# Optimization experiments

Measured on AMD Instinct MI355X. Metric: run time of the kernel, lower is better.

The kernel has to match this reference:

```python
import jax, jax.numpy as jnp
import numpy as np

TAU = 2.0
V_TH = 1.0


def setup_inputs() -> dict:
    key = jax.random.key(0)
    k1, k2, k3 = jax.random.split(key, 3)
    T, B, H = 128, 64, 1024
    x = jax.random.normal(k1, (T, B, H), dtype=jnp.float32)
    # nn.Linear(H, H, bias=False) weights, shape [out, in]
    W1 = jax.random.normal(k2, (H, H), dtype=jnp.float32) / np.sqrt(H)
    W2 = jax.random.normal(k3, (H, H), dtype=jnp.float32) / np.sqrt(H)
    return {"x": x, "W1": W1, "W2": W2}


def _lif_scan(x_proj):
    # x_proj: [T, B, H]; membrane v starts at 0.
    def step(v, xt):
        h = v + (xt - v) / TAU          # leaky integrate
        s = (h >= V_TH).astype(h.dtype)  # hard-threshold spike
        v_new = h * (1.0 - s)            # soft reset (to 0 on spike)
        return v_new, s

    v0 = jnp.zeros(x_proj.shape[1:], dtype=x_proj.dtype)
    _, spikes = jax.lax.scan(step, v0, x_proj)
    return spikes  # [T, B, H]


def reference(x, W1, W2):
    # fc1 applied per timestep == one batched GEMM over [T*B, H]
    x_proj = jnp.einsum('tbh,oh->tbo', x, W1)
    spike = _lif_scan(x_proj)
    out = jnp.einsum('tbh,oh->tbo', spike, W2)
    return out
```

## Files before the change

kernel.cpp:

```cpp
#include <hip/hip_runtime.h>
#include <hip/hip_bf16.h>
#include <stdint.h>

#define TT 128
#define BB 64
#define HH 1024
#define MM (TT * BB)
#define NLANE (BB * HH)
#define DELTA 1.0e-4
#define F16_ONE 0x3C00

typedef __attribute__((ext_vector_type(8))) short bf16x8;
typedef __attribute__((ext_vector_type(8))) _Float16 f16x8;
typedef __attribute__((ext_vector_type(4))) float f32x4;

#define GLOAD16(g, l)                                                        \
    __builtin_amdgcn_global_load_lds(                                        \
        (const __attribute__((address_space(1))) unsigned int*)(g),          \
        (__attribute__((address_space(3))) unsigned int*)(l), 16, 0, 0)

#define FENCE() __builtin_amdgcn_sched_barrier(0)

static __device__ __forceinline__ unsigned short bf16_bits(float f) {
    __hip_bfloat16 b = __float2bfloat16(f);
    return *reinterpret_cast<unsigned short*>(&b);
}
static __device__ __forceinline__ unsigned short f16_bits(float f) {
    _Float16 h = (_Float16)f;
    return *reinterpret_cast<unsigned short*>(&h);
}

__global__ __launch_bounds__(256) void prep_fused(const float* __restrict__ x,
                                                  const float* __restrict__ W1,
                                                  const float* __restrict__ W2,
                                                  unsigned short* __restrict__ A2,
                                                  unsigned short* __restrict__ B2,
                                                  unsigned short* __restrict__ w2h,
                                                  int* __restrict__ cnt) {
    const int bid = blockIdx.x;
    if (bid == 0 && threadIdx.x == 0) *cnt = 0;

    if (bid < 9216) {
        const bool isX = (bid < 8192);
        const int i = (isX ? bid : bid - 8192) * 256 + threadIdx.x;
        const float4 v4 = reinterpret_cast<const float4*>(isX ? x : W1)[i];
        float v[4] = {v4.x, v4.y, v4.z, v4.w};
        unsigned short hb[4], lb[4];
#pragma unroll
        for (int c = 0; c < 4; c++) {
            hb[c] = bf16_bits(v[c]);
            __hip_bfloat16 hh = *reinterpret_cast<__hip_bfloat16*>(&hb[c]);
            lb[c] = bf16_bits(v[c] - __bfloat162float(hh));
        }
        ushort4* dst = reinterpret_cast<ushort4*>(isX ? A2 : B2);
        const int r = i >> 8;
        const int c4 = i & 255;
        dst[(size_t)r * 512 + c4]       = make_ushort4(hb[0], hb[1], hb[2], hb[3]);
        dst[(size_t)r * 512 + 256 + c4] = make_ushort4(lb[0], lb[1], lb[2], lb[3]);
    } else {
        const int i = (bid - 9216) * 256 + threadIdx.x;
        const float4 v4 = reinterpret_cast<const float4*>(W2)[i];
        float v[4] = {v4.x, v4.y, v4.z, v4.w};
        unsigned short hb[4];
#pragma unroll
        for (int c = 0; c < 4; c++) hb[c] = f16_bits(v[c]);
        reinterpret_cast<ushort4*>(w2h)[i] = make_ushort4(hb[0], hb[1], hb[2], hb[3]);
    }
}

__global__ __launch_bounds__(512, 2) void gemm1_8ph(const unsigned short* __restrict__ A2,
                                                    const unsigned short* __restrict__ B2,
                                                    float* __restrict__ C) {
    __shared__ short As_[2][256 * 64];
    __shared__ short Bs_[2][128 * 64];

    const int tid = threadIdx.x;
    const int lane = tid & 63;
    const int wave = tid >> 6;
    const int wr = wave >> 2;
    const int wc = wave & 3;

    const int bid = blockIdx.x;
    const int orig = (bid & 7) * 32 + (bid >> 3);
    const int m0 = (orig >> 3) * 256;
    const int n0 = (orig & 7) * 128;

    const int rsel = lane & 15;
    const int part = lane >> 4;

    int adrA[8][2], adrB[2][2];
#pragma unroll
    for (int mi = 0; mi < 8; mi++) {
        const int ra = wr * 128 + mi * 16 + rsel;
#pragma unroll
        for (int ks = 0; ks < 2; ks++) {
            const int slot = ks * 4 + part;
            adrA[mi][ks] = ra * 64 + ((slot ^ (ra & 7)) << 3);
        }
    }
#pragma unroll
    for (int ni = 0; ni < 2; ni++) {
        const int rb = wc * 32 + ni * 16 + rsel;
#pragma unroll
        for (int ks = 0; ks < 2; ks++) {
            const int slot = ks * 4 + part;
            adrB[ni][ks] = rb * 64 + ((slot ^ (rb & 7)) << 3);
        }
    }

    const int srow = tid >> 3;
    const int gslot8 = ((tid & 7) ^ (srow & 7)) << 3;
    const int ldso = wave * 512;

#define STAGE_A(buf, q, kcol)                                                     \
    GLOAD16(&A2[(size_t)(m0 + (q) * 64 + srow) * 2048 + (kcol) + gslot8],         \
            &As_[buf][(q) * 4096 + ldso])
#define STAGE_B(buf, b, kcol)                                                     \
    GLOAD16(&B2[(size_t)(n0 + (b) * 64 + srow) * 2048 + (kcol) + gslot8],         \
            &Bs_[buf][(b) * 4096 + ldso])

#define KA_OF(t) (((t) < 16) ? (t) * 64 : (t) * 64 - 1024)
#define KB_OF(t) (((t) < 32) ? (t) * 64 : (t) * 64 - 2048)

    STAGE_A(0, 0, 0); STAGE_A(0, 2, 0);
    STAGE_B(0, 0, 0); STAGE_B(0, 1, 0);
    STAGE_A(0, 1, 0); STAGE_A(0, 3, 0);
    STAGE_B(1, 0, 64); STAGE_B(1, 1, 64);
    STAGE_A(1, 0, 64); STAGE_A(1, 2, 64);
    asm volatile("s_waitcnt vmcnt(6)" ::: "memory");
    FENCE();
    __builtin_amdgcn_s_barrier();
    FENCE();

    f32x4 acc[8][2] = {};

    for (int t = 0; t < 48; ++t) {
        const short* As = As_[t & 1];
        const short* Bs = Bs_[t & 1];
        const int t1 = t + 1, t2 = t + 2;
        const int kA1 = KA_OF(t1);
        const int kA2 = KA_OF(t2);
        const int kB2 = KB_OF(t2);

        bf16x8 a[4][2], b[2][2];

#pragma unroll
        for (int mi = 0; mi < 4; mi++)
#pragma unroll
            for (int ks = 0; ks < 2; ks++)
                a[mi][ks] = *reinterpret_cast<const bf16x8*>(&As[adrA[mi][ks]]);
#pragma unroll
        for (int ni = 0; ni < 2; ni++)
#pragma unroll
            for (int ks = 0; ks < 2; ks++)
                b[ni][ks] = *reinterpret_cast<const bf16x8*>(&Bs[adrB[ni][ks]]);
        STAGE_A((t1 & 1), 1, kA1);
        STAGE_A((t1 & 1), 3, kA1);
        FENCE();
        __builtin_amdgcn_s_barrier();
        FENCE();
        __builtin_amdgcn_s_setprio(1);
#pragma unroll
        for (int mi = 0; mi < 4; mi++)
#pragma unroll
            for (int ni = 0; ni < 2; ni++) {
                acc[mi][ni] = __builtin_amdgcn_mfma_f32_16x16x32_bf16(a[mi][0], b[ni][0], acc[mi][ni], 0, 0, 0);
                acc[mi][ni] = __builtin_amdgcn_mfma_f32_16x16x32_bf16(a[mi][1], b[ni][1], acc[mi][ni], 0, 0, 0);
            }
        __builtin_amdgcn_s_setprio(0);
        asm volatile("s_waitcnt vmcnt(6)" ::: "memory");
        FENCE();
        __builtin_amdgcn_s_barrier();
        FENCE();

#pragma unroll
        for (int mi = 0; mi < 4; mi++)
#pragma unroll
            for (int ks = 0; ks < 2; ks++)
                a[mi][ks] = *reinterpret_cast<const bf16x8*>(&As[adrA[mi + 4][ks]]);
        STAGE_B((t & 1), 0, kB2);
        STAGE_B((t & 1), 1, kB2);
        STAGE_A((t & 1), 0, kA2);
        STAGE_A((t & 1), 2, kA2);
        FENCE();
        __builtin_amdgcn_s_barrier();
        FENCE();
        __builtin_amdgcn_s_setprio(1);
#pragma unroll
        for (int mi = 0; mi < 4; mi++)
#pragma unroll
            for (int ni = 0; ni < 2; ni++) {
                acc[mi + 4][ni] = __builtin_amdgcn_mfma_f32_16x16x32_bf16(a[mi][0], b[ni][0], acc[mi + 4][ni], 0, 0, 0);
                acc[mi + 4][ni] = __builtin_amdgcn_mfma_f32_16x16x32_bf16(a[mi][1], b[ni][1], acc[mi + 4][ni], 0, 0, 0);
            }
        __builtin_amdgcn_s_setprio(0);
        asm volatile("s_waitcnt vmcnt(6)" ::: "memory");
        FENCE();
        __builtin_amdgcn_s_barrier();
        FENCE();
    }
#undef STAGE_A
#undef STAGE_B

    const int col = lane & 15;
    const int quad = lane >> 4;
#pragma unroll
    for (int mi = 0; mi < 8; mi++)
#pragma unroll
        for (int ni = 0; ni < 2; ni++) {
            const int m = m0 + wr * 128 + mi * 16 + quad * 4;
            const int n = n0 + wc * 32 + ni * 16 + col;
            float* dst = &C[(size_t)m * HH + n];
#pragma unroll
            for (int r = 0; r < 4; r++)
                dst[(size_t)r * HH] = acc[mi][ni][r];
        }
}

__global__ __launch_bounds__(256) void lif_scan_flag(const float* __restrict__ xp,
                                                     unsigned short* __restrict__ sp,
                                                     int* __restrict__ count,
                                                     int* __restrict__ list) {
    const int idx = blockIdx.x * 256 + threadIdx.x;
    double v = 0.0;
    bool flg = false;
#pragma unroll 4
    for (int t = 0; t < TT; t++) {
        const double x = (double)xp[(size_t)t * NLANE + idx];
        const double h = v + (x - v) * 0.5;
        const bool s = (h >= 1.0);
        flg |= (fabs(h - 1.0) < DELTA);
        v = s ? 0.0 : h;
        sp[(size_t)t * NLANE + idx] = s ? (unsigned short)F16_ONE : (unsigned short)0;
    }
    if (flg) {
        const int i = atomicAdd(count, 1);
        list[i] = idx;
    }
}

__global__ __launch_bounds__(1024) void recompute_fused(const float* __restrict__ X,
                                                        const float* __restrict__ W1,
                                                        const int* __restrict__ count,
                                                        const int* __restrict__ list,
                                                        unsigned short* __restrict__ sp) {
    __shared__ double hbuf[TT];
    const int cnt = *count;
    const int wv = threadIdx.x >> 6;
    const int ln = threadIdx.x & 63;

    for (int li = blockIdx.x; li < cnt; li += gridDim.x) {
        const int lane = list[li];
        const int b = lane >> 10;
        const int h = lane & (HH - 1);
        const float4* w4 = reinterpret_cast<const float4*>(W1 + (size_t)h * HH);

        for (int t = wv; t < TT; t += 16) {
            const float4* x4 = reinterpret_cast<const float4*>(X + (size_t)(t * BB + b) * HH);
            double s0 = 0.0, s1 = 0.0, s2 = 0.0, s3 = 0.0;
#pragma unroll
            for (int i = 0; i < 4; i++) {
                const float4 xa = x4[ln + i * 64];
                const float4 wa = w4[ln + i * 64];
                s0 = fma((double)xa.x, (double)wa.x, s0);
                s1 = fma((double)xa.y, (double)wa.y, s1);
                s2 = fma((double)xa.z, (double)wa.z, s2);
                s3 = fma((double)xa.w, (double)wa.w, s3);
            }
            double s = (s0 + s1) + (s2 + s3);
#pragma unroll
            for (int off = 32; off >= 1; off >>= 1)
                s += __shfl_down(s, off);
            if (ln == 0) hbuf[t] = s;
        }
        __syncthreads();

        if (threadIdx.x == 0) {
            double v = 0.0;
            for (int t = 0; t < TT; t++) {
                const double hh = v + (hbuf[t] - v) * 0.5;
                const bool s = (hh >= 1.0);
                v = s ? 0.0 : hh;
                sp[(size_t)t * NLANE + lane] = s ? (unsigned short)F16_ONE : (unsigned short)0;
            }
        }
        __syncthreads();
    }
}

__global__ __launch_bounds__(256) void gemm2_mfma(const unsigned short* __restrict__ S,
                                                  const unsigned short* __restrict__ W,
                                                  float* __restrict__ O) {
    __shared__ short As[128 * 32];
    __shared__ short Bs[64 * 32];

    const int tid = threadIdx.x;
    const int lane = tid & 63;
    const int wave = tid >> 6;
    const int m0 = blockIdx.y * 128;
    const int n0 = blockIdx.x * 64;
    const int wm = (wave >> 1) * 64;
    const int wn = (wave & 1) * 32;

    const int rsel = lane & 15;
    const int part = lane >> 4;

    int adrA[4], adrB[2];
#pragma unroll
    for (int i = 0; i < 4; i++) {
        const int ra = wm + i * 16 + rsel;
        adrA[i] = ra * 32 + (part ^ ((ra >> 1) & 3)) * 8;
    }
#pragma unroll
    for (int i = 0; i < 2; i++) {
        const int rb = wn + i * 16 + rsel;
        adrB[i] = rb * 32 + (part ^ ((rb >> 1) & 3)) * 8;
    }

    f32x4 acc[4][2] = {};

    for (int k0 = 0; k0 < HH; k0 += 32) {
#pragma unroll
        for (int p = 0; p < 3; p++) {
            const int c = tid + p * 256;
            const int cb = wave * 64 + p * 256;
            if (c < 512) {
                const int row = c >> 2;
                const int pslot = c & 3;
                const int pdata = pslot ^ ((row >> 1) & 3);
                GLOAD16(&S[(size_t)(m0 + row) * HH + k0 + pdata * 8], &As[cb * 8]);
            } else {
                const int c2 = c - 512;
                const int row = c2 >> 2;
                const int pslot = c2 & 3;
                const int pdata = pslot ^ ((row >> 1) & 3);
                GLOAD16(&W[(size_t)(n0 + row) * HH + k0 + pdata * 8], &Bs[(cb - 512) * 8]);
            }
        }
        __syncthreads();

        f16x8 a[4], b[2];
#pragma unroll
        for (int mi = 0; mi < 4; mi++)
            a[mi] = *reinterpret_cast<f16x8*>(&As[adrA[mi]]);
#pragma unroll
        for (int ni = 0; ni < 2; ni++)
            b[ni] = *reinterpret_cast<f16x8*>(&Bs[adrB[ni]]);

#pragma unroll
        for (int mi = 0; mi < 4; mi++)
#pragma unroll
            for (int ni = 0; ni < 2; ni++)
                acc[mi][ni] = __builtin_amdgcn_mfma_f32_16x16x32_f16(
                    a[mi], b[ni], acc[mi][ni], 0, 0, 0);

        __syncthreads();
    }

    const int col = lane & 15;
    const int quad = lane >> 4;
#pragma unroll
    for (int mi = 0; mi < 4; mi++)
#pragma unroll
        for (int ni = 0; ni < 2; ni++) {
            const int m = m0 + wm + mi * 16 + quad * 4;
            const int n = n0 + wn + ni * 16 + col;
            float* dst = &O[(size_t)m * HH + n];
#pragma unroll
            for (int r = 0; r < 4; r++)
                dst[(size_t)r * HH] = acc[mi][ni][r];
        }
}

extern "C" void kernel_launch(void* const* d_in, const int* in_sizes, int n_in,
                              void* d_out, int out_size, void* d_ws, size_t ws_size,
                              hipStream_t stream) {
    const float* x  = (const float*)d_in[0];
    const float* W1 = (const float*)d_in[1];
    const float* W2 = (const float*)d_in[2];
    float* out = (float*)d_out;

    char* ws = (char*)d_ws;

    unsigned short* A2   = (unsigned short*)ws;
    unsigned short* B2   = A2 + (size_t)MM * 2048;
    unsigned short* w2h  = B2 + (size_t)HH * 2048;
    int*            list = (int*)(w2h + (size_t)HH * HH);
    int*            cnt  = list + NLANE;
    float*          xp   = (float*)(((uintptr_t)(cnt + 64) + 255) & ~(uintptr_t)255);
    unsigned short* sp   = (unsigned short*)ws;

    prep_fused<<<10240, 256, 0, stream>>>(x, W1, W2, A2, B2, w2h, cnt);

    gemm1_8ph<<<256, 512, 0, stream>>>(A2, B2, xp);

    lif_scan_flag<<<NLANE / 256, 256, 0, stream>>>(xp, sp, cnt, list);

    recompute_fused<<<512, 1024, 0, stream>>>(x, W1, cnt, list, sp);

    dim3 g2(HH / 64, MM / 128);
    gemm2_mfma<<<g2, 256, 0, stream>>>(sp, w2h, out);
}
```

Measured before the change: 217.4 us.

## Triple-buffer GEMM1 LDS with one barrier per step and 64x64 wave tiles

Rewrites the first GEMM's main loop to use three LDS buffers instead of two. The next-but-one K-tile is prefetched while the current one is consumed, so only one workgroup barrier is needed per iteration instead of four. The wave layout changes from 2x4 to 4x2, so each wave computes a 64x64 tile with 4 A and 4 B fragments. This raises the MFMA-to-LDS-read ratio. In exchange LDS use grows to about 147KB per block, and the tail iterations issue redundant clamped prefetches.

```diff
diff --git a/kernel.cpp b/kernel.cpp
--- a/kernel.cpp
+++ b/kernel.cpp
@@ -68,17 +68,17 @@
     }
 }
 
-__global__ __launch_bounds__(512, 2) void gemm1_8ph(const unsigned short* __restrict__ A2,
-                                                    const unsigned short* __restrict__ B2,
-                                                    float* __restrict__ C) {
-    __shared__ short As_[2][256 * 64];
-    __shared__ short Bs_[2][128 * 64];
+__global__ __launch_bounds__(512, 2) void gemm1_tb(const unsigned short* __restrict__ A2,
+                                                   const unsigned short* __restrict__ B2,
+                                                   float* __restrict__ C) {
+    __shared__ short As_[3][256 * 64];
+    __shared__ short Bs_[3][128 * 64];
 
     const int tid = threadIdx.x;
     const int lane = tid & 63;
     const int wave = tid >> 6;
-    const int wr = wave >> 2;
-    const int wc = wave & 3;
+    const int wr = wave >> 1;
+    const int wc = wave & 1;
 
     const int bid = blockIdx.x;
     const int orig = (bid & 7) * 32 + (bid >> 3);
@@ -88,10 +88,10 @@
     const int rsel = lane & 15;
     const int part = lane >> 4;
 
-    int adrA[8][2], adrB[2][2];
-#pragma unroll
-    for (int mi = 0; mi < 8; mi++) {
-        const int ra = wr * 128 + mi * 16 + rsel;
+    int adrA[4][2], adrB[4][2];
+#pragma unroll
+    for (int mi = 0; mi < 4; mi++) {
+        const int ra = wr * 64 + mi * 16 + rsel;
 #pragma unroll
         for (int ks = 0; ks < 2; ks++) {
             const int slot = ks * 4 + part;
@@ -99,8 +99,8 @@
         }
     }
 #pragma unroll
-    for (int ni = 0; ni < 2; ni++) {
-        const int rb = wc * 32 + ni * 16 + rsel;
+    for (int ni = 0; ni < 4; ni++) {
+        const int rb = wc * 64 + ni * 16 + rsel;
 #pragma unroll
         for (int ks = 0; ks < 2; ks++) {
             const int slot = ks * 4 + part;
@@ -122,94 +122,82 @@
 #define KA_OF(t) (((t) < 16) ? (t) * 64 : (t) * 64 - 1024)
 #define KB_OF(t) (((t) < 32) ? (t) * 64 : (t) * 64 - 2048)
 
-    STAGE_A(0, 0, 0); STAGE_A(0, 2, 0);
+    STAGE_A(0, 0, 0); STAGE_A(0, 1, 0); STAGE_A(0, 2, 0); STAGE_A(0, 3, 0);
     STAGE_B(0, 0, 0); STAGE_B(0, 1, 0);
-    STAGE_A(0, 1, 0); STAGE_A(0, 3, 0);
+    STAGE_A(1, 0, 64); STAGE_A(1, 1, 64); STAGE_A(1, 2, 64); STAGE_A(1, 3, 64);
     STAGE_B(1, 0, 64); STAGE_B(1, 1, 64);
-    STAGE_A(1, 0, 64); STAGE_A(1, 2, 64);
     asm volatile("s_waitcnt vmcnt(6)" ::: "memory");
     FENCE();
     __builtin_amdgcn_s_barrier();
     FENCE();
 
-    f32x4 acc[8][2] = {};
+    f32x4 acc[4][4] = {};
+    int bufr = 0;
 
     for (int t = 0; t < 48; ++t) {
-        const short* As = As_[t & 1];
-        const short* Bs = Bs_[t & 1];
-        const int t1 = t + 1, t2 = t + 2;
-        const int kA1 = KA_OF(t1);
-        const int kA2 = KA_OF(t2);
-        const int kB2 = KB_OF(t2);
-
-        bf16x8 a[4][2], b[2][2];
-
-#pragma unroll
-        for (int mi = 0; mi < 4; mi++)
-#pragma unroll
-            for (int ks = 0; ks < 2; ks++)
-                a[mi][ks] = *reinterpret_cast<const bf16x8*>(&As[adrA[mi][ks]]);
-#pragma unroll
-        for (int ni = 0; ni < 2; ni++)
-#pragma unroll
-            for (int ks = 0; ks < 2; ks++)
-                b[ni][ks] = *reinterpret_cast<const bf16x8*>(&Bs[adrB[ni][ks]]);
-        STAGE_A((t1 & 1), 1, kA1);
-        STAGE_A((t1 & 1), 3, kA1);
-        FENCE();
-        __builtin_amdgcn_s_barrier();
-        FENCE();
+        const short* As = As_[bufr];
+        const short* Bs = Bs_[bufr];
+        int sbuf = bufr + 2; if (sbuf >= 3) sbuf -= 3;
+        const int tc = (t + 2 < 48) ? t + 2 : 47;
+        const int kA2 = KA_OF(tc);
+        const int kB2 = KB_OF(tc);
+
+        bf16x8 a[4], b[4];
+
+#pragma unroll
+        for (int mi = 0; mi < 4; mi++)
+            a[mi] = *reinterpret_cast<const bf16x8*>(&As[adrA[mi][0]]);
+#pragma unroll
+        for (int ni = 0; ni < 4; ni++)
+            b[ni] = *reinterpret_cast<const bf16x8*>(&Bs[adrB[ni][0]]);
+        STAGE_A(sbuf, 0, kA2);
+        STAGE_A(sbuf, 1, kA2);
+        STAGE_B(sbuf, 0, kB2);
         __builtin_amdgcn_s_setprio(1);
 #pragma unroll
         for (int mi = 0; mi < 4; mi++)
 #pragma unroll
-            for (int ni = 0; ni < 2; ni++) {
-                acc[mi][ni] = __builtin_amdgcn_mfma_f32_16x16x32_bf16(a[mi][0], b[ni][0], acc[mi][ni], 0, 0, 0);
-                acc[mi][ni] = __builtin_amdgcn_mfma_f32_16x16x32_bf16(a[mi][1], b[ni][1], acc[mi][ni], 0, 0, 0);
-            }
+            for (int ni = 0; ni < 4; ni++)
+                acc[mi][ni] = __builtin_amdgcn_mfma_f32_16x16x32_bf16(a[mi], b[ni], acc[mi][ni], 0, 0, 0);
         __builtin_amdgcn_s_setprio(0);
+
+#pragma unroll
+        for (int mi = 0; mi < 4; mi++)
+            a[mi] = *reinterpret_cast<const bf16x8*>(&As[adrA[mi][1]]);
+#pragma unroll
+        for (int ni = 0; ni < 4; ni++)
+            b[ni] = *reinterpret_cast<const bf16x8*>(&Bs[adrB[ni][1]]);
+        STAGE_A(sbuf, 2, kA2);
+        STAGE_A(sbuf, 3, kA2);
+        STAGE_B(sbuf, 1, kB2);
+        __builtin_amdgcn_s_setprio(1);
+#pragma unroll
+        for (int mi = 0; mi < 4; mi++)
+#pragma unroll
+            for (int ni = 0; ni < 4; ni++)
+                acc[mi][ni] = __builtin_amdgcn_mfma_f32_16x16x32_bf16(a[mi], b[ni], acc[mi][ni], 0, 0, 0);
+        __builtin_amdgcn_s_setprio(0);
+
         asm volatile("s_waitcnt vmcnt(6)" ::: "memory");
         FENCE();
         __builtin_amdgcn_s_barrier();
         FENCE();
 
-#pragma unroll
-        for (int mi = 0; mi < 4; mi++)
-#pragma unroll
-            for (int ks = 0; ks < 2; ks++)
-                a[mi][ks] = *reinterpret_cast<const bf16x8*>(&As[adrA[mi + 4][ks]]);
-        STAGE_B((t & 1), 0, kB2);
-        STAGE_B((t & 1), 1, kB2);
-        STAGE_A((t & 1), 0, kA2);
-        STAGE_A((t & 1), 2, kA2);
-        FENCE();
-        __builtin_amdgcn_s_barrier();
-        FENCE();
-        __builtin_amdgcn_s_setprio(1);
-#pragma unroll
-        for (int mi = 0; mi < 4; mi++)
-#pragma unroll
-            for (int ni = 0; ni < 2; ni++) {
-                acc[mi + 4][ni] = __builtin_amdgcn_mfma_f32_16x16x32_bf16(a[mi][0], b[ni][0], acc[mi + 4][ni], 0, 0, 0);
-                acc[mi + 4][ni] = __builtin_amdgcn_mfma_f32_16x16x32_bf16(a[mi][1], b[ni][1], acc[mi + 4][ni], 0, 0, 0);
-            }
-        __builtin_amdgcn_s_setprio(0);
-        asm volatile("s_waitcnt vmcnt(6)" ::: "memory");
-        FENCE();
-        __builtin_amdgcn_s_barrier();
-        FENCE();
+        bufr = (bufr == 2) ? 0 : bufr + 1;
     }
 #undef STAGE_A
 #undef STAGE_B
 
+    asm volatile("s_waitcnt vmcnt(0)" ::: "memory");
+
     const int col = lane & 15;
     const int quad = lane >> 4;
 #pragma unroll
-    for (int mi = 0; mi < 8; mi++)
-#pragma unroll
-        for (int ni = 0; ni < 2; ni++) {
-            const int m = m0 + wr * 128 + mi * 16 + quad * 4;
-            const int n = n0 + wc * 32 + ni * 16 + col;
+    for (int mi = 0; mi < 4; mi++)
+#pragma unroll
+        for (int ni = 0; ni < 4; ni++) {
+            const int m = m0 + wr * 64 + mi * 16 + quad * 4;
+            const int n = n0 + wc * 64 + ni * 16 + col;
             float* dst = &C[(size_t)m * HH + n];
 #pragma unroll
             for (int r = 0; r < 4; r++)
@@ -392,7 +380,7 @@
 
     prep_fused<<<10240, 256, 0, stream>>>(x, W1, W2, A2, B2, w2h, cnt);
 
-    gemm1_8ph<<<256, 512, 0, stream>>>(A2, B2, xp);
+    gemm1_tb<<<256, 512, 0, stream>>>(A2, B2, xp);
 
     lif_scan_flag<<<NLANE / 256, 256, 0, stream>>>(xp, sp, cnt, list);
 
```

Result: no change. 214.6 us (-1.3%).
